# Optimization experiments

Measured on AMD Instinct MI355X. Metric: run time of the kernel, lower is better.

The kernel has to match this reference:

```python
import jax, jax.numpy as jnp
import numpy as np

N, E, F, H, S, L, B = 20000, 320000, 64, 256, 32, 128, 16
TAU = 1.0
EPS = 1e-9


def _glorot(k, i, o):
    return (jax.random.normal(k, (i, o), jnp.float32) / np.sqrt(i)).astype(jnp.float32)


def _mlp3(h, w1, b1, w2, b2, w3, b3):
    h = jax.nn.relu(h @ w1 + b1)
    h = jax.nn.relu(h @ w2 + b2)
    return h @ w3 + b3


def _gnn_layer(x, src, dst, w1, b1, w2, b2, w3, b3):
    # PyG: x_i = x[dst] (target), x_j = x[src] (source); aggregate 'add' at target
    m = _mlp3(jnp.concatenate([x[dst], x[src]], axis=1), w1, b1, w2, b2, w3, b3)  # [E, H]
    return jax.ops.segment_sum(m, dst, num_segments=N)  # [N, H]


def _layer_norm(x, g, b):
    mu = x.mean(-1, keepdims=True)
    var = ((x - mu) ** 2).mean(-1, keepdims=True)
    return (x - mu) * jax.lax.rsqrt(var + 1e-5) * g + b


def setup_inputs() -> dict:
    key = jax.random.key(0)
    ks = jax.random.split(key, 32)
    d = {
        'x': jax.random.normal(ks[0], (N, F), jnp.float32),
        'u': jax.random.uniform(ks[1], (N, S), jnp.float32, minval=1e-6, maxval=1.0 - 1e-6),
        'edge_index': jax.random.randint(ks[2], (2, E), 0, N, jnp.int32),
        'batch': jnp.sort(jax.random.randint(ks[3], (N,), 0, B, jnp.int32)),
        # gnn1 MLP: 2F -> H -> H -> H
        'g1w1': _glorot(ks[4], 2 * F, H), 'g1b1': jnp.zeros((H,), jnp.float32),
        'g1w2': _glorot(ks[5], H, H),     'g1b2': jnp.zeros((H,), jnp.float32),
        'g1w3': _glorot(ks[6], H, H),     'g1b3': jnp.zeros((H,), jnp.float32),
        'ln1g': jnp.ones((H,), jnp.float32), 'ln1b': jnp.zeros((H,), jnp.float32),
        # gnn2 MLP: 2H -> H -> H -> H
        'g2w1': _glorot(ks[7], 2 * H, H), 'g2b1': jnp.zeros((H,), jnp.float32),
        'g2w2': _glorot(ks[8], H, H),     'g2b2': jnp.zeros((H,), jnp.float32),
        'g2w3': _glorot(ks[9], H, H),     'g2b3': jnp.zeros((H,), jnp.float32),
        'ln2g': jnp.ones((H,), jnp.float32), 'ln2b': jnp.zeros((H,), jnp.float32),
        # assignment MLP: H -> H -> S
        'aw1': _glorot(ks[10], H, H), 'ab1': jnp.zeros((H,), jnp.float32),
        'aw2': _glorot(ks[11], H, S), 'ab2': jnp.zeros((S,), jnp.float32),
        # output MLP: H -> H -> L
        'ow1': _glorot(ks[12], H, H), 'ob1': jnp.zeros((H,), jnp.float32),
        'ow2': _glorot(ks[13], H, L), 'ob2': jnp.zeros((L,), jnp.float32),
    }
    return d


def reference(x, u, edge_index, batch,
              g1w1, g1b1, g1w2, g1b2, g1w3, g1b3, ln1g, ln1b,
              g2w1, g2b1, g2w2, g2b2, g2w3, g2b3, ln2g, ln2b,
              aw1, ab1, aw2, ab2, ow1, ob1, ow2, ob2):
    src, dst = edge_index[0], edge_index[1]
    x = _layer_norm(jax.nn.relu(_gnn_layer(x, src, dst, g1w1, g1b1, g1w2, g1b2, g1w3, g1b3)), ln1g, ln1b)
    x = _layer_norm(jax.nn.relu(_gnn_layer(x, src, dst, g2w1, g2b1, g2w2, g2b2, g2w3, g2b3)), ln2g, ln2b)
    # Hierarchical pooling with Gumbel-softmax (soft, tau=1.0); u is the uniform noise
    logits = jax.nn.relu(x @ aw1 + ab1) @ aw2 + ab2  # [N, S]
    g = -jnp.log(-jnp.log(u + EPS) + EPS)
    s = jax.nn.softmax((logits + g) / TAU, axis=-1)  # [N, S]
    entropy = -jnp.mean(jnp.sum(s * jnp.log(s + EPS), axis=1))
    avg_s = s.mean(axis=0)
    diversity = jnp.sum(avg_s * jnp.log(avg_s + EPS))
    assign_loss = entropy + diversity
    xe = x[:, None, :] * s[:, :, None]  # [N, S, H]
    pooled = jax.ops.segment_sum(xe, batch, num_segments=B)  # [B, S, H]
    latent = jax.nn.relu(pooled @ ow1 + ob1) @ ow2 + ob2  # [B, S, L]
    return (latent, s, assign_loss)
```

## Files before the change

### kernel.cpp

```cpp
#include <hip/hip_runtime.h>
#include <stdint.h>

#define NN 20000
#define NE 320000
#define NBATCH 16
#define NTILE 2500

typedef short short8 __attribute__((ext_vector_type(8)));
typedef float f32x4  __attribute__((ext_vector_type(4)));

__device__ __forceinline__ unsigned short f2bf(float f) {
  union { float f; unsigned u; } v; v.f = f;
  unsigned r = v.u + 0x7FFFu + ((v.u >> 16) & 1u);
  return (unsigned short)(r >> 16);
}
__device__ __forceinline__ float bf2f(unsigned short h) {
  union { unsigned u; float f; } v; v.u = ((unsigned)h) << 16;
  return v.f;
}
__device__ __forceinline__ float bf2fs(short h) { return bf2f((unsigned short)h); }

__device__ __forceinline__ unsigned cvt_pk_bf16(float lo, float hi) {
  unsigned r;
  asm("v_cvt_pk_bf16_f32 %0, %1, %2" : "=v"(r) : "v"(lo), "v"(hi));
  return r;
}

#define HOFF(e, k) (((e) << 8) + (((((k) >> 3) ^ ((e) & 7)) << 3) + ((k) & 7)))
#define HK(e, k, KT) ((e) * (KT) + (((((k) >> 3) ^ ((e) & 7)) << 3) + ((k) & 7)))

struct TD { const float* s; unsigned short* d; int R, C, r0, ld; };
struct TDs { TD t[13]; };

__global__ void wprep(TDs all, const int* __restrict__ dstI, int* __restrict__ deg) {
  if (blockIdx.y == 13) {
    int stride = gridDim.x * blockDim.x;
    for (int e = blockIdx.x * blockDim.x + threadIdx.x; e < NE; e += stride)
      atomicAdd(&deg[dstI[e]], 1);
    return;
  }
  TD td = all.t[blockIdx.y];
  int stride = gridDim.x * blockDim.x;
  int i0 = blockIdx.x * blockDim.x + threadIdx.x;
  if (td.ld == 0) {
    for (int i = i0; i < td.R; i += stride) td.d[i] = f2bf(td.s[i]);
  } else {
    int total = td.R * td.C;
    for (int i = i0; i < total; i += stride) {
      int c = i / td.R;
      int r = i - c * td.R;
      td.d[i] = f2bf(td.s[(size_t)(td.r0 + r) * td.ld + c]);
    }
  }
}

__global__ void scan_bounds(const int* __restrict__ deg, int* __restrict__ rowstart,
                            int* __restrict__ cursor, const int* __restrict__ batch,
                            int* __restrict__ bstart,
                            const float* __restrict__ g1b1, const float* __restrict__ g2b1,
                            float* __restrict__ b1cat1, float* __restrict__ b1cat2) {
  if (blockIdx.x == 0) {
    __shared__ int part[256];
    int t = threadIdx.x;
    int c0 = t * 80; if (c0 > NN) c0 = NN;
    int c1 = c0 + 80; if (c1 > NN) c1 = NN;
    int s = 0;
    for (int i = c0; i < c1; ++i) s += deg[i];
    part[t] = s;
    __syncthreads();
    if (t == 0) {
      int run = 0;
      for (int i = 0; i < 256; ++i) { int v = part[i]; part[i] = run; run += v; }
    }
    __syncthreads();
    int run = part[t];
    for (int i = c0; i < c1; ++i) { rowstart[i] = run; cursor[i] = run; run += deg[i]; }
    if (t == 255) rowstart[NN] = run;
  } else if (blockIdx.x == 80) {
    int t = threadIdx.x;
    b1cat1[t] = g1b1[t]; b1cat1[256 + t] = 0.f;
    b1cat2[t] = g2b1[t]; b1cat2[256 + t] = 0.f;
  } else {
    int n = (blockIdx.x - 1) * 256 + threadIdx.x;
    if (n >= NN) return;
    int bn = batch[n];
    if (n == 0) {
      for (int b2 = 0; b2 <= bn; ++b2) bstart[b2] = 0;
    } else {
      int bp = batch[n - 1];
      for (int b2 = bp + 1; b2 <= bn; ++b2) bstart[b2] = n;
    }
    if (n == NN - 1) {
      for (int b2 = bn + 1; b2 <= NBATCH; ++b2) bstart[b2] = NN;
    }
  }
}

__global__ void fillcsr(const int* __restrict__ srcI, const int* __restrict__ dstI,
                        int* __restrict__ cursor, int* __restrict__ sSrc,
                        int* __restrict__ sDst) {
  int e = blockIdx.x * 256 + threadIdx.x;
  if (e < NE) {
    int d = dstI[e];
    int slot = atomicAdd(&cursor[d], 1);
    sDst[slot] = d;
    sSrc[slot] = srcI[e];
  }
}

template <int KT>
__global__ __launch_bounds__(512, 4) void gemmTs(
    const unsigned short* __restrict__ WT, const unsigned short* __restrict__ In,
    const float* __restrict__ bias, unsigned short* __restrict__ Out,
    int M, int Nout, int ldo) {
  __shared__ __align__(16) unsigned short h[128 * KT];
  const int tid = threadIdx.x;
  const int rb0 = blockIdx.y * 128;
  {
    int r = tid & 127;
    int rg = rb0 + r; if (rg >= M) rg = M - 1;
    const unsigned short* src = In + (size_t)rg * KT + (tid >> 7) * (KT / 4);
    int c0 = (tid >> 7) * (KT / 4);
#pragma unroll
    for (int i = 0; i < KT / 32; ++i) {
      short8 v = *(const short8*)(src + i * 8);
      *(short8*)&h[HK(r, c0 + i * 8, KT)] = v;
    }
  }
  __syncthreads();

  const int lane = tid & 63, w = tid >> 6;
  const int wf = w >> 1, we = w & 1;
  const int l15 = lane & 15, q = lane >> 4;
  const int fb = blockIdx.x * 256 + wf * 64;
  const int rb = rb0 + we * 64;
  f32x4 acc[4][4] = {};
  const short8 zz = {0, 0, 0, 0, 0, 0, 0, 0};
  for (int kc = 0; kc < KT; kc += 32) {
    short8 a[4], bq[4];
#pragma unroll
    for (int i = 0; i < 4; ++i) {
      if (fb + i * 16 < Nout)
        a[i] = *(const short8*)(WT + (size_t)(fb + i * 16 + l15) * KT + kc + q * 8);
      else
        a[i] = zz;
      bq[i] = *(const short8*)&h[HK(we * 64 + i * 16 + l15, kc + q * 8, KT)];
    }
#pragma unroll
    for (int i = 0; i < 4; ++i)
#pragma unroll
      for (int j = 0; j < 4; ++j)
        acc[i][j] = __builtin_amdgcn_mfma_f32_16x16x32_bf16(a[i], bq[j], acc[i][j], 0, 0, 0);
  }
#pragma unroll
  for (int i = 0; i < 4; ++i) {
    int f0 = fb + i * 16 + q * 4;
    if (f0 >= Nout) continue;
    float4 bs = make_float4(0.f, 0.f, 0.f, 0.f);
    if (bias) bs = *(const float4*)(bias + f0);
#pragma unroll
    for (int j = 0; j < 4; ++j) {
      int r = rb + j * 16 + l15;
      if (r >= M) continue;
      uint2 o = make_uint2(cvt_pk_bf16(acc[i][j][0] + bs.x, acc[i][j][1] + bs.y),
                           cvt_pk_bf16(acc[i][j][2] + bs.z, acc[i][j][3] + bs.w));
      *(uint2*)(Out + (size_t)r * ldo + f0) = o;
    }
  }
}

__global__ __launch_bounds__(512, 4) void edge_h2agg(
    const unsigned short* __restrict__ PQ, const int* __restrict__ sSrc,
    const int* __restrict__ sDst,
    const unsigned short* __restrict__ W2T, const float* __restrict__ b2,
    int* __restrict__ segcnt, int* __restrict__ segbuf, float* __restrict__ agg) {
  __shared__ __align__(16) unsigned short h[128 * 256];
  const int tid = threadIdx.x;
  const int e0 = blockIdx.x * 128;

  {
    int r = tid & 127;
    int c0 = (tid >> 7) * 64;
    int dn = sDst[e0 + r];
    int sn = sSrc[e0 + r];
    const unsigned short* pd = PQ + (size_t)dn * 512 + c0;
    const unsigned short* ps = PQ + (size_t)sn * 512 + 256 + c0;
#pragma unroll
    for (int i = 0; i < 8; ++i) {
      short8 dv = *(const short8*)(pd + i * 8);
      short8 sv = *(const short8*)(ps + i * 8);
      float a0 = fmaxf(bf2fs(dv[0]) + bf2fs(sv[0]), 0.f);
      float a1 = fmaxf(bf2fs(dv[1]) + bf2fs(sv[1]), 0.f);
      float a2 = fmaxf(bf2fs(dv[2]) + bf2fs(sv[2]), 0.f);
      float a3 = fmaxf(bf2fs(dv[3]) + bf2fs(sv[3]), 0.f);
      float a4 = fmaxf(bf2fs(dv[4]) + bf2fs(sv[4]), 0.f);
      float a5 = fmaxf(bf2fs(dv[5]) + bf2fs(sv[5]), 0.f);
      float a6 = fmaxf(bf2fs(dv[6]) + bf2fs(sv[6]), 0.f);
      float a7 = fmaxf(bf2fs(dv[7]) + bf2fs(sv[7]), 0.f);
      uint4 o = make_uint4(cvt_pk_bf16(a0, a1), cvt_pk_bf16(a2, a3),
                           cvt_pk_bf16(a4, a5), cvt_pk_bf16(a6, a7));
      *(uint4*)&h[HOFF(r, c0 + i * 8)] = o;
    }
  }
  __syncthreads();

  const int lane = tid & 63, w = tid >> 6;
  const int wf = w >> 1, we = w & 1;
  const int l15 = lane & 15, q = lane >> 4;
  const int fb = wf * 64, eb = we * 64;
  f32x4 acc[4][4];

#pragma unroll
  for (int i = 0; i < 4; ++i)
#pragma unroll
    for (int j = 0; j < 4; ++j) { f32x4 z = {0.f, 0.f, 0.f, 0.f}; acc[i][j] = z; }
  for (int kc = 0; kc < 256; kc += 32) {
    short8 a[4], bq[4];
#pragma unroll
    for (int i = 0; i < 4; ++i)
      a[i] = *(const short8*)(W2T + (size_t)(fb + i * 16 + l15) * 256 + kc + q * 8);
#pragma unroll
    for (int j = 0; j < 4; ++j)
      bq[j] = *(const short8*)&h[HOFF(eb + j * 16 + l15, kc + q * 8)];
#pragma unroll
    for (int i = 0; i < 4; ++i)
#pragma unroll
      for (int j = 0; j < 4; ++j)
        acc[i][j] = __builtin_amdgcn_mfma_f32_16x16x32_bf16(a[i], bq[j], acc[i][j], 0, 0, 0);
  }
  __syncthreads();
#pragma unroll
  for (int i = 0; i < 4; ++i) {
    int f0 = fb + i * 16 + q * 4;
    float4 bs = *(const float4*)(b2 + f0);
#pragma unroll
    for (int j = 0; j < 4; ++j) {
      int e = eb + j * 16 + l15;
      float v0 = fmaxf(acc[i][j][0] + bs.x, 0.f);
      float v1 = fmaxf(acc[i][j][1] + bs.y, 0.f);
      float v2 = fmaxf(acc[i][j][2] + bs.z, 0.f);
      float v3 = fmaxf(acc[i][j][3] + bs.w, 0.f);
      uint2 o = make_uint2(cvt_pk_bf16(v0, v1), cvt_pk_bf16(v2, v3));
      *(uint2*)&h[HOFF(e, f0)] = o;
    }
  }
  if (tid < 128) {
    int d0 = sDst[e0 + tid];
    bool flag = (tid == 0) || (sDst[e0 + tid - 1] != d0);
    if (flag) {
      int idx = atomicAdd(&segcnt[blockIdx.x], 1);
      segbuf[blockIdx.x * 128 + idx] = tid;
    }
  }
  __syncthreads();

  {
    int cnt = segcnt[blockIdx.x];
    int f4 = (tid & 63) * 4;
    int sg = tid >> 6;
    const int* sb = segbuf + blockIdx.x * 128;
    for (int k = sg; k < cnt; k += 8) {
      int start = sb[k];
      int end = 128;
      for (int j2 = 0; j2 < cnt; ++j2) {
        int v = sb[j2];
        if (v > start && v < end) end = v;
      }
      int node = sDst[e0 + start];
      float s0 = 0.f, s1 = 0.f, s2 = 0.f, s3 = 0.f;
      for (int rr = start; rr < end; ++rr) {
        ushort4 v = *(const ushort4*)&h[HOFF(rr, f4)];
        s0 += bf2f(v.x); s1 += bf2f(v.y); s2 += bf2f(v.z); s3 += bf2f(v.w);
      }
      float* pr = agg + (size_t)node * 256 + f4;
      if (start == 0 || end == 128) {
        atomicAdd(pr + 0, s0); atomicAdd(pr + 1, s1);
        atomicAdd(pr + 2, s2); atomicAdd(pr + 3, s3);
      } else {
        *(float4*)pr = make_float4(s0, s1, s2, s3);
      }
    }
  }
}

__global__ __launch_bounds__(512, 4) void node_gemm(
    const unsigned short* __restrict__ W3T, const float* __restrict__ aggH2,
    const float* __restrict__ b3, const int* __restrict__ deg,
    float* __restrict__ outm) {
  __shared__ __align__(16) unsigned short h[128 * 256];
  const int tid = threadIdx.x;
  const int rb0 = blockIdx.x * 128;
  {
    int r = tid & 127;
    int rg = rb0 + r; if (rg >= NN) rg = NN - 1;
    int c0 = (tid >> 7) * 64;
    const float* src = aggH2 + (size_t)rg * 256 + c0;
#pragma unroll
    for (int i = 0; i < 8; ++i) {
      float4 lo = *(const float4*)(src + i * 8);
      float4 hi = *(const float4*)(src + i * 8 + 4);
      uint4 o = make_uint4(cvt_pk_bf16(lo.x, lo.y), cvt_pk_bf16(lo.z, lo.w),
                           cvt_pk_bf16(hi.x, hi.y), cvt_pk_bf16(hi.z, hi.w));
      *(uint4*)&h[HOFF(r, c0 + i * 8)] = o;
    }
  }
  __syncthreads();

  const int lane = tid & 63, w = tid >> 6;
  const int wf = w >> 1, we = w & 1;
  const int l15 = lane & 15, q = lane >> 4;
  const int fb = wf * 64;
  const int rb = rb0 + we * 64;
  f32x4 acc[4][4] = {};
  for (int kc = 0; kc < 256; kc += 32) {
    short8 a[4], bq[4];
#pragma unroll
    for (int i = 0; i < 4; ++i) {
      a[i] = *(const short8*)(W3T + (size_t)(fb + i * 16 + l15) * 256 + kc + q * 8);
      bq[i] = *(const short8*)&h[HOFF(we * 64 + i * 16 + l15, kc + q * 8)];
    }
#pragma unroll
    for (int i = 0; i < 4; ++i)
#pragma unroll
      for (int j = 0; j < 4; ++j)
        acc[i][j] = __builtin_amdgcn_mfma_f32_16x16x32_bf16(a[i], bq[j], acc[i][j], 0, 0, 0);
  }
#pragma unroll
  for (int i = 0; i < 4; ++i) {
    int f0 = fb + i * 16 + q * 4;
    float4 b3v = *(const float4*)(b3 + f0);
#pragma unroll
    for (int j = 0; j < 4; ++j) {
      int r = rb + j * 16 + l15;
      if (r >= NN) continue;
      float dg = (float)deg[r];
      *(float4*)(outm + (size_t)r * 256 + f0) =
          make_float4(acc[i][j][0] + dg * b3v.x, acc[i][j][1] + dg * b3v.y,
                      acc[i][j][2] + dg * b3v.z, acc[i][j][3] + dg * b3v.w);
    }
  }
}

__global__ void relu_ln(const float* __restrict__ agg, const float* __restrict__ g,
                        const float* __restrict__ b, unsigned short* __restrict__ out) {
  int row = blockIdx.x * 4 + (threadIdx.x >> 6);
  int lane = threadIdx.x & 63;
  if (row >= NN) return;
  float4 v = *(const float4*)(agg + (size_t)row * 256 + lane * 4);
  v.x = fmaxf(v.x, 0.f); v.y = fmaxf(v.y, 0.f); v.z = fmaxf(v.z, 0.f); v.w = fmaxf(v.w, 0.f);
  float s = v.x + v.y + v.z + v.w;
  float sq = v.x * v.x + v.y * v.y + v.z * v.z + v.w * v.w;
  for (int off = 32; off >= 1; off >>= 1) {
    s += __shfl_xor(s, off);
    sq += __shfl_xor(sq, off);
  }
  float mu = s * (1.f / 256.f);
  float var = sq * (1.f / 256.f) - mu * mu;
  float rs = rsqrtf(var + 1e-5f);
  float4 gg = *(const float4*)(g + lane * 4);
  float4 bb = *(const float4*)(b + lane * 4);
  ushort4 o;
  o.x = f2bf((v.x - mu) * rs * gg.x + bb.x);
  o.y = f2bf((v.y - mu) * rs * gg.y + bb.y);
  o.z = f2bf((v.z - mu) * rs * gg.z + bb.z);
  o.w = f2bf((v.w - mu) * rs * gg.w + bb.w);
  *(ushort4*)(out + (size_t)row * 256 + lane * 4) = o;
}

__global__ __launch_bounds__(512, 4) void assign_gumbel(
    const unsigned short* __restrict__ x2b, const unsigned short* __restrict__ aw1T,
    const float* __restrict__ ab1, const unsigned short* __restrict__ aw2T,
    const float* __restrict__ ab2, const float* __restrict__ u,
    float* __restrict__ sf, float* __restrict__ entacc, float* __restrict__ avgacc) {
  __shared__ __align__(16) unsigned short sh[64 * 256];
  __shared__ float sh_logit[64 * 33];
  __shared__ float lavg[32];
  __shared__ float lent;
  const int tid = threadIdx.x;
  const int n0 = blockIdx.x * 64;
  if (tid < 32) lavg[tid] = 0.f;
  if (tid == 0) lent = 0.f;

  const int lane = tid & 63, w = tid >> 6;
  const int l15 = lane & 15, q = lane >> 4;

  {
    const int wf = w >> 1, we = w & 1;
    const int fb = wf * 64, eb = we * 32;
    f32x4 acc[4][2];
#pragma unroll
    for (int i = 0; i < 4; ++i)
#pragma unroll
      for (int j = 0; j < 2; ++j) { f32x4 z = {0.f, 0.f, 0.f, 0.f}; acc[i][j] = z; }
    for (int kc = 0; kc < 256; kc += 32) {
      short8 a[4], bq[2];
#pragma unroll
      for (int i = 0; i < 4; ++i)
        a[i] = *(const short8*)(aw1T + (size_t)(fb + i * 16 + l15) * 256 + kc + q * 8);
#pragma unroll
      for (int j = 0; j < 2; ++j) {
        int rr = n0 + eb + j * 16 + l15;
        if (rr >= NN) rr = NN - 1;
        bq[j] = *(const short8*)(x2b + (size_t)rr * 256 + kc + q * 8);
      }
#pragma unroll
      for (int i = 0; i < 4; ++i)
#pragma unroll
        for (int j = 0; j < 2; ++j)
          acc[i][j] = __builtin_amdgcn_mfma_f32_16x16x32_bf16(a[i], bq[j], acc[i][j], 0, 0, 0);
    }
#pragma unroll
    for (int i = 0; i < 4; ++i) {
      int f0 = fb + i * 16 + q * 4;
      float4 bs = *(const float4*)(ab1 + f0);
#pragma unroll
      for (int j = 0; j < 2; ++j) {
        int e = eb + j * 16 + l15;
        ushort4 o;
        o.x = f2bf(fmaxf(acc[i][j][0] + bs.x, 0.f));
        o.y = f2bf(fmaxf(acc[i][j][1] + bs.y, 0.f));
        o.z = f2bf(fmaxf(acc[i][j][2] + bs.z, 0.f));
        o.w = f2bf(fmaxf(acc[i][j][3] + bs.w, 0.f));
        *(ushort4*)&sh[HOFF(e, f0)] = o;
      }
    }
  }
  __syncthreads();

  {
    const int rg = w & 3, fg = w >> 2;
    if (fg < 2) {
      f32x4 acc = {0.f, 0.f, 0.f, 0.f};
      for (int kc = 0; kc < 256; kc += 32) {
        short8 a = *(const short8*)(aw2T + (size_t)(fg * 16 + l15) * 256 + kc + q * 8);
        short8 bq = *(const short8*)&sh[HOFF(rg * 16 + l15, kc + q * 8)];
        acc = __builtin_amdgcn_mfma_f32_16x16x32_bf16(a, bq, acc, 0, 0, 0);
      }
      int rowL = rg * 16 + l15;
#pragma unroll
      for (int t2 = 0; t2 < 4; ++t2) {
        int f = fg * 16 + q * 4 + t2;
        sh_logit[rowL * 33 + f] = acc[t2] + ab2[f];
      }
    }
  }
  __syncthreads();

  if (tid < 256) {
    int rowL = tid >> 2, sub = tid & 3;
    int n = n0 + rowL;
    if (n < NN) {
      int j0 = sub * 8;
      float z[8];
      float4 u0 = *(const float4*)(u + (size_t)n * 32 + j0);
      float4 u1 = *(const float4*)(u + (size_t)n * 32 + j0 + 4);
      float uu[8] = {u0.x, u0.y, u0.z, u0.w, u1.x, u1.y, u1.z, u1.w};
      float m = -1e30f;
#pragma unroll
      for (int j = 0; j < 8; ++j) {
        z[j] = sh_logit[rowL * 33 + j0 + j] - logf(-logf(uu[j] + 1e-9f) + 1e-9f);
        m = fmaxf(m, z[j]);
      }
      m = fmaxf(m, __shfl_xor(m, 1));
      m = fmaxf(m, __shfl_xor(m, 2));
      float sum = 0.f;
#pragma unroll
      for (int j = 0; j < 8; ++j) { z[j] = expf(z[j] - m); sum += z[j]; }
      sum += __shfl_xor(sum, 1);
      sum += __shfl_xor(sum, 2);
      float inv = 1.f / sum;
      float ent = 0.f;
      float so[8];
#pragma unroll
      for (int j = 0; j < 8; ++j) {
        float sj = z[j] * inv;
        so[j] = sj;
        ent += sj * logf(sj + 1e-9f);
        atomicAdd(&lavg[j0 + j], sj);
      }
      *(float4*)(sf + (size_t)n * 32 + j0) = make_float4(so[0], so[1], so[2], so[3]);
      *(float4*)(sf + (size_t)n * 32 + j0 + 4) = make_float4(so[4], so[5], so[6], so[7]);
      ent += __shfl_xor(ent, 1);
      ent += __shfl_xor(ent, 2);
      if (sub == 0) atomicAdd(&lent, ent);
    }
  }
  __syncthreads();
  if (tid < 32) atomicAdd(&avgacc[tid], lavg[tid]);
  if (tid == 0) atomicAdd(entacc, lent);
}

__global__ __launch_bounds__(512, 4) void pool_part(
    const unsigned short* __restrict__ x2b, const float* __restrict__ sf,
    const int* __restrict__ bstart, float* __restrict__ part) {
  const int b = blockIdx.x, ci = blockIdx.y;
  const int n0b = bstart[b], n1b = bstart[b + 1];
  const int t = threadIdx.x;
  const int si = t >> 4;
  const int h0 = (t & 15) * 16;
  float acc[16];
#pragma unroll
  for (int k = 0; k < 16; ++k) acc[k] = 0.f;
  for (int nst = n0b + ci * 64; nst < n1b; nst += 16 * 64) {
    int nend = (nst + 64 < n1b) ? nst + 64 : n1b;
    for (int n = nst; n < nend; ++n) {
      float sv = sf[(size_t)n * 32 + si];
      const unsigned short* xr = x2b + (size_t)n * 256 + h0;
      short8 x0 = *(const short8*)xr;
      short8 x1 = *(const short8*)(xr + 8);
#pragma unroll
      for (int j = 0; j < 8; ++j) acc[j] = fmaf(sv, bf2fs(x0[j]), acc[j]);
#pragma unroll
      for (int j = 0; j < 8; ++j) acc[8 + j] = fmaf(sv, bf2fs(x1[j]), acc[8 + j]);
    }
  }
  float* pp = part + (((size_t)b * 16 + ci) << 13) + si * 256 + h0;
#pragma unroll
  for (int k = 0; k < 16; k += 4)
    *(float4*)(pp + k) = make_float4(acc[k], acc[k + 1], acc[k + 2], acc[k + 3]);
}

__global__ void pool_reduce(const float* __restrict__ part, float* __restrict__ pooled) {
  int g = blockIdx.x * 256 + threadIdx.x;
  int b = g >> 13, rem = g & 8191;
  const float* p = part + (((size_t)b * 16) << 13) + rem;
  float s = 0.f;
#pragma unroll
  for (int c = 0; c < 16; ++c) s += p[(size_t)c << 13];
  pooled[g] = s;
}

__global__ __launch_bounds__(512, 4) void out_mlp(
    const float* __restrict__ pooled, const unsigned short* __restrict__ ow1T,
    const float* __restrict__ ob1, const unsigned short* __restrict__ ow2T,
    const float* __restrict__ ob2, float* __restrict__ latent,
    const float* __restrict__ accs, float* __restrict__ outloss) {
  __shared__ __align__(16) unsigned short sh[64 * 256];
  const int tid = threadIdx.x;
  const int n0 = blockIdx.x * 64;
  const int lane = tid & 63, w = tid >> 6;
  const int l15 = lane & 15, q = lane >> 4;

  if (blockIdx.x == 0 && tid < 64) {
    float d = 0.f;
    if (tid < 32) {
      float a = accs[16 + tid] * (1.f / NN);
      d = a * logf(a + 1e-9f);
    }
    for (int off = 32; off >= 1; off >>= 1) d += __shfl_xor(d, off);
    if (tid == 0) outloss[0] = -accs[0] * (1.f / NN) + d;
  }

  {
    const int wf = w >> 1, we = w & 1;
    const int fb = wf * 64, eb = we * 32;
    f32x4 acc[4][2];
#pragma unroll
    for (int i = 0; i < 4; ++i)
#pragma unroll
      for (int j = 0; j < 2; ++j) { f32x4 z = {0.f, 0.f, 0.f, 0.f}; acc[i][j] = z; }
    for (int kc = 0; kc < 256; kc += 32) {
      short8 a[4], bq[2];
#pragma unroll
      for (int i = 0; i < 4; ++i)
        a[i] = *(const short8*)(ow1T + (size_t)(fb + i * 16 + l15) * 256 + kc + q * 8);
#pragma unroll
      for (int j = 0; j < 2; ++j) {
        int rr = n0 + eb + j * 16 + l15;
        const float* pr = pooled + (size_t)rr * 256 + kc + q * 8;
        float4 lo = *(const float4*)pr;
        float4 hi = *(const float4*)(pr + 4);
        short8 o;
        o[0] = (short)f2bf(lo.x); o[1] = (short)f2bf(lo.y);
        o[2] = (short)f2bf(lo.z); o[3] = (short)f2bf(lo.w);
        o[4] = (short)f2bf(hi.x); o[5] = (short)f2bf(hi.y);
        o[6] = (short)f2bf(hi.z); o[7] = (short)f2bf(hi.w);
        bq[j] = o;
      }
#pragma unroll
      for (int i = 0; i < 4; ++i)
#pragma unroll
        for (int j = 0; j < 2; ++j)
          acc[i][j] = __builtin_amdgcn_mfma_f32_16x16x32_bf16(a[i], bq[j], acc[i][j], 0, 0, 0);
    }
#pragma unroll
    for (int i = 0; i < 4; ++i) {
      int f0 = fb + i * 16 + q * 4;
      float4 bs = *(const float4*)(ob1 + f0);
#pragma unroll
      for (int j = 0; j < 2; ++j) {
        int e = eb + j * 16 + l15;
        ushort4 o;
        o.x = f2bf(fmaxf(acc[i][j][0] + bs.x, 0.f));
        o.y = f2bf(fmaxf(acc[i][j][1] + bs.y, 0.f));
        o.z = f2bf(fmaxf(acc[i][j][2] + bs.z, 0.f));
        o.w = f2bf(fmaxf(acc[i][j][3] + bs.w, 0.f));
        *(ushort4*)&sh[HOFF(e, f0)] = o;
      }
    }
  }
  __syncthreads();

  {
    const int wf = w >> 1, we = w & 1;
    const int fb = wf * 32, eb = we * 32;
    f32x4 acc[2][2];
#pragma unroll
    for (int i = 0; i < 2; ++i)
#pragma unroll
      for (int j = 0; j < 2; ++j) { f32x4 z = {0.f, 0.f, 0.f, 0.f}; acc[i][j] = z; }
    for (int kc = 0; kc < 256; kc += 32) {
      short8 a[2], bq[2];
#pragma unroll
      for (int i = 0; i < 2; ++i)
        a[i] = *(const short8*)(ow2T + (size_t)(fb + i * 16 + l15) * 256 + kc + q * 8);
#pragma unroll
      for (int j = 0; j < 2; ++j)
        bq[j] = *(const short8*)&sh[HOFF(eb + j * 16 + l15, kc + q * 8)];
#pragma unroll
      for (int i = 0; i < 2; ++i)
#pragma unroll
        for (int j = 0; j < 2; ++j)
          acc[i][j] = __builtin_amdgcn_mfma_f32_16x16x32_bf16(a[i], bq[j], acc[i][j], 0, 0, 0);
    }
#pragma unroll
    for (int i = 0; i < 2; ++i) {
      int f0 = fb + i * 16 + q * 4;
      float4 bs = *(const float4*)(ob2 + f0);
#pragma unroll
      for (int j = 0; j < 2; ++j) {
        int rr = n0 + eb + j * 16 + l15;
        *(float4*)(latent + (size_t)rr * 128 + f0) =
            make_float4(acc[i][j][0] + bs.x, acc[i][j][1] + bs.y,
                        acc[i][j][2] + bs.z, acc[i][j][3] + bs.w);
      }
    }
  }
}

extern "C" void kernel_launch(void* const* d_in, const int* in_sizes, int n_in,
                              void* d_out, int out_size, void* d_ws, size_t ws_size,
                              hipStream_t stream) {
  (void)in_sizes; (void)n_in; (void)out_size; (void)ws_size;
  const float* x = (const float*)d_in[0];
  const float* u = (const float*)d_in[1];
  const int* ei = (const int*)d_in[2];
  const int* batch = (const int*)d_in[3];
  const float* g1w1 = (const float*)d_in[4];
  const float* g1b1 = (const float*)d_in[5];
  const float* g1w2 = (const float*)d_in[6];
  const float* g1b2 = (const float*)d_in[7];
  const float* g1w3 = (const float*)d_in[8];
  const float* g1b3 = (const float*)d_in[9];
  const float* ln1g = (const float*)d_in[10];
  const float* ln1b = (const float*)d_in[11];
  const float* g2w1 = (const float*)d_in[12];
  const float* g2b1 = (const float*)d_in[13];
  const float* g2w2 = (const float*)d_in[14];
  const float* g2b2 = (const float*)d_in[15];
  const float* g2w3 = (const float*)d_in[16];
  const float* g2b3 = (const float*)d_in[17];
  const float* ln2g = (const float*)d_in[18];
  const float* ln2b = (const float*)d_in[19];
  const float* aw1 = (const float*)d_in[20];
  const float* ab1 = (const float*)d_in[21];
  const float* aw2 = (const float*)d_in[22];
  const float* ab2 = (const float*)d_in[23];
  const float* ow1 = (const float*)d_in[24];
  const float* ob1 = (const float*)d_in[25];
  const float* ow2 = (const float*)d_in[26];
  const float* ob2 = (const float*)d_in[27];
  const int* srcI = ei;
  const int* dstI = ei + NE;

  char* wp = (char*)d_ws;
  size_t off = 0;
  auto alloc = [&](size_t bytes) {
    void* p = wp + off;
    off += (bytes + 255) & ~(size_t)255;
    return p;
  };
  unsigned short* W1catT = (unsigned short*)alloc((size_t)512 * 64 * 2);
  unsigned short* W2catT = (unsigned short*)alloc((size_t)512 * 256 * 2);
  unsigned short* g1w2T = (unsigned short*)alloc((size_t)256 * 256 * 2);
  unsigned short* g1w3T = (unsigned short*)alloc((size_t)256 * 256 * 2);
  unsigned short* g2w2T = (unsigned short*)alloc((size_t)256 * 256 * 2);
  unsigned short* g2w3T = (unsigned short*)alloc((size_t)256 * 256 * 2);
  unsigned short* aw1T = (unsigned short*)alloc((size_t)256 * 256 * 2);
  unsigned short* aw2T = (unsigned short*)alloc((size_t)32 * 256 * 2);
  unsigned short* ow1T = (unsigned short*)alloc((size_t)256 * 256 * 2);
  unsigned short* ow2T = (unsigned short*)alloc((size_t)128 * 256 * 2);
  unsigned short* xb = (unsigned short*)alloc((size_t)NN * 64 * 2);
  unsigned short* PQ = (unsigned short*)alloc((size_t)NN * 512 * 2);
  unsigned short* x1b = (unsigned short*)alloc((size_t)NN * 256 * 2);
  unsigned short* x2b = (unsigned short*)alloc((size_t)NN * 256 * 2);
  int* bstart = (int*)alloc(32 * 4);
  int* cursor = (int*)alloc((size_t)NN * 4);
  int* rowstart = (int*)alloc((size_t)(NN + 1) * 4);
  int* sSrc = (int*)alloc((size_t)NE * 4);
  int* sDst = (int*)alloc((size_t)NE * 4);
  int* segbuf = (int*)alloc((size_t)2 * NTILE * 128 * 4);
  float* b1cat1 = (float*)alloc(512 * 4);
  float* b1cat2 = (float*)alloc(512 * 4);
  char* zbase = (char*)(wp + off);
  float* accs = (float*)alloc(64 * 4);
  float* pooled = (float*)alloc((size_t)512 * 256 * 4);
  int* deg = (int*)alloc((size_t)NN * 4);
  int* segcnt = (int*)alloc((size_t)2 * NTILE * 4);
  float* agg1 = (float*)alloc((size_t)NN * 256 * 4);
  float* agg2 = (float*)alloc((size_t)NN * 256 * 4);
  size_t zbytes = (size_t)((char*)(wp + off) - zbase);

  float* aggm = (float*)PQ;
  float* poolpart = agg1;

  float* out_f = (float*)d_out;
  float* out_latent = out_f;
  float* out_s = out_f + 65536;
  float* out_loss = out_f + 65536 + 640000;

  TDs tds;
  tds.t[0] = {g1w1, W1catT, 64, 256, 0, 256};
  tds.t[1] = {g1w1, W1catT + 256 * 64, 64, 256, 64, 256};
  tds.t[2] = {g1w2, g1w2T, 256, 256, 0, 256};
  tds.t[3] = {g1w3, g1w3T, 256, 256, 0, 256};
  tds.t[4] = {g2w1, W2catT, 256, 256, 0, 256};
  tds.t[5] = {g2w1, W2catT + 256 * 256, 256, 256, 256, 256};
  tds.t[6] = {g2w2, g2w2T, 256, 256, 0, 256};
  tds.t[7] = {g2w3, g2w3T, 256, 256, 0, 256};
  tds.t[8] = {aw1, aw1T, 256, 256, 0, 256};
  tds.t[9] = {aw2, aw2T, 256, 32, 0, 32};
  tds.t[10] = {ow1, ow1T, 256, 256, 0, 256};
  tds.t[11] = {ow2, ow2T, 256, 128, 0, 128};
  tds.t[12] = {x, xb, NN * 64, 1, 0, 0};

  (void)hipMemsetAsync(zbase, 0, zbytes, stream);
  wprep<<<dim3(128, 14), 256, 0, stream>>>(tds, dstI, deg);

  scan_bounds<<<dim3(81), 256, 0, stream>>>(deg, rowstart, cursor, batch, bstart,
                                            g1b1, g2b1, b1cat1, b1cat2);
  fillcsr<<<dim3(1250), 256, 0, stream>>>(srcI, dstI, cursor, sSrc, sDst);

  gemmTs<64><<<dim3(2, 157), 512, 0, stream>>>(W1catT, xb, b1cat1, PQ, NN, 512, 512);
  edge_h2agg<<<dim3(NTILE), 512, 0, stream>>>(PQ, sSrc, sDst, g1w2T, g1b2,
                                              segcnt, segbuf, agg1);
  node_gemm<<<dim3(157), 512, 0, stream>>>(g1w3T, agg1, g1b3, deg, aggm);
  relu_ln<<<dim3(5000), 256, 0, stream>>>(aggm, ln1g, ln1b, x1b);

  gemmTs<256><<<dim3(2, 157), 512, 0, stream>>>(W2catT, x1b, b1cat2, PQ, NN, 512, 512);
  edge_h2agg<<<dim3(NTILE), 512, 0, stream>>>(PQ, sSrc, sDst, g2w2T, g2b2,
                                              segcnt + NTILE, segbuf + (size_t)NTILE * 128, agg2);
  node_gemm<<<dim3(157), 512, 0, stream>>>(g2w3T, agg2, g2b3, deg, aggm);
  relu_ln<<<dim3(5000), 256, 0, stream>>>(aggm, ln2g, ln2b, x2b);

  assign_gumbel<<<dim3(313), 512, 0, stream>>>(x2b, aw1T, ab1, aw2T, ab2, u,
                                               out_s, accs, accs + 16);

  pool_part<<<dim3(16, 16), 512, 0, stream>>>(x2b, out_s, bstart, poolpart);
  pool_reduce<<<dim3(512), 256, 0, stream>>>(poolpart, pooled);

  out_mlp<<<dim3(8), 512, 0, stream>>>(pooled, ow1T, ob1, ow2T, ob2, out_latent,
                                       accs, out_loss);
}
```

Before: 679.4 us.

## Process two edge tiles per block with register-resident weights and prefetched gathers

The edge MLP+aggregation kernel now handles two 128-edge tiles per block. It keeps the W2 weight fragments in registers across both tiles and prefetches the next tile's PQ gathers while the current tile runs its MFMA. Segment bookkeeping moves from global atomics and buffers into shared memory, which removes the segcnt/segbuf allocations. The cost is much higher register pressure (128 VGPRs of weights plus the prefetch registers), which may lower occupancy under launch_bounds(512,4) or cause spills.

```diff
diff --git a/kernel.cpp b/kernel.cpp
--- a/kernel.cpp
+++ b/kernel.cpp
@@ -4,7 +4,8 @@
 #define NN 20000
 #define NE 320000
 #define NBATCH 16
-#define NTILE 2500
+#define EB_TPB 2
+#define EB_GRID 1250
 
 typedef short short8 __attribute__((ext_vector_type(8)));
 typedef float f32x4  __attribute__((ext_vector_type(4)));
@@ -173,113 +174,137 @@
     const unsigned short* __restrict__ PQ, const int* __restrict__ sSrc,
     const int* __restrict__ sDst,
     const unsigned short* __restrict__ W2T, const float* __restrict__ b2,
-    int* __restrict__ segcnt, int* __restrict__ segbuf, float* __restrict__ agg) {
+    float* __restrict__ agg) {
   __shared__ __align__(16) unsigned short h[128 * 256];
+  __shared__ int seg_s[129];
   const int tid = threadIdx.x;
-  const int e0 = blockIdx.x * 128;
-
-  {
-    int r = tid & 127;
-    int c0 = (tid >> 7) * 64;
-    int dn = sDst[e0 + r];
-    int sn = sSrc[e0 + r];
-    const unsigned short* pd = PQ + (size_t)dn * 512 + c0;
-    const unsigned short* ps = PQ + (size_t)sn * 512 + 256 + c0;
-#pragma unroll
-    for (int i = 0; i < 8; ++i) {
-      short8 dv = *(const short8*)(pd + i * 8);
-      short8 sv = *(const short8*)(ps + i * 8);
-      float a0 = fmaxf(bf2fs(dv[0]) + bf2fs(sv[0]), 0.f);
-      float a1 = fmaxf(bf2fs(dv[1]) + bf2fs(sv[1]), 0.f);
-      float a2 = fmaxf(bf2fs(dv[2]) + bf2fs(sv[2]), 0.f);
-      float a3 = fmaxf(bf2fs(dv[3]) + bf2fs(sv[3]), 0.f);
-      float a4 = fmaxf(bf2fs(dv[4]) + bf2fs(sv[4]), 0.f);
-      float a5 = fmaxf(bf2fs(dv[5]) + bf2fs(sv[5]), 0.f);
-      float a6 = fmaxf(bf2fs(dv[6]) + bf2fs(sv[6]), 0.f);
-      float a7 = fmaxf(bf2fs(dv[7]) + bf2fs(sv[7]), 0.f);
-      uint4 o = make_uint4(cvt_pk_bf16(a0, a1), cvt_pk_bf16(a2, a3),
-                           cvt_pk_bf16(a4, a5), cvt_pk_bf16(a6, a7));
-      *(uint4*)&h[HOFF(r, c0 + i * 8)] = o;
-    }
-  }
-  __syncthreads();
-
   const int lane = tid & 63, w = tid >> 6;
   const int wf = w >> 1, we = w & 1;
   const int l15 = lane & 15, q = lane >> 4;
   const int fb = wf * 64, eb = we * 64;
-  f32x4 acc[4][4];
-
+  const int r = tid & 127;
+  const int c0 = (tid >> 7) * 64;
+  const int e0 = blockIdx.x * (128 * EB_TPB);
+
+  short8 wa[4][8];
 #pragma unroll
   for (int i = 0; i < 4; ++i)
 #pragma unroll
-    for (int j = 0; j < 4; ++j) { f32x4 z = {0.f, 0.f, 0.f, 0.f}; acc[i][j] = z; }
-  for (int kc = 0; kc < 256; kc += 32) {
-    short8 a[4], bq[4];
+    for (int kk = 0; kk < 8; ++kk)
+      wa[i][kk] = *(const short8*)(W2T + (size_t)(fb + i * 16 + l15) * 256 + kk * 32 + q * 8);
+
+  short8 dv[8], sv[8];
+  {
+    int dn = sDst[e0 + r], sn = sSrc[e0 + r];
+    const unsigned short* pd = PQ + (size_t)dn * 512 + c0;
+    const unsigned short* ps = PQ + (size_t)sn * 512 + 256 + c0;
+#pragma unroll
+    for (int i = 0; i < 8; ++i) {
+      dv[i] = *(const short8*)(pd + i * 8);
+      sv[i] = *(const short8*)(ps + i * 8);
+    }
+  }
+
+  for (int t = 0; t < EB_TPB; ++t) {
+    const int te0 = e0 + t * 128;
+#pragma unroll
+    for (int i = 0; i < 8; ++i) {
+      float a0 = fmaxf(bf2fs(dv[i][0]) + bf2fs(sv[i][0]), 0.f);
+      float a1 = fmaxf(bf2fs(dv[i][1]) + bf2fs(sv[i][1]), 0.f);
+      float a2 = fmaxf(bf2fs(dv[i][2]) + bf2fs(sv[i][2]), 0.f);
+      float a3 = fmaxf(bf2fs(dv[i][3]) + bf2fs(sv[i][3]), 0.f);
+      float a4 = fmaxf(bf2fs(dv[i][4]) + bf2fs(sv[i][4]), 0.f);
+      float a5 = fmaxf(bf2fs(dv[i][5]) + bf2fs(sv[i][5]), 0.f);
+      float a6 = fmaxf(bf2fs(dv[i][6]) + bf2fs(sv[i][6]), 0.f);
+      float a7 = fmaxf(bf2fs(dv[i][7]) + bf2fs(sv[i][7]), 0.f);
+      uint4 o = make_uint4(cvt_pk_bf16(a0, a1), cvt_pk_bf16(a2, a3),
+                           cvt_pk_bf16(a4, a5), cvt_pk_bf16(a6, a7));
+      *(uint4*)&h[HOFF(r, c0 + i * 8)] = o;
+    }
+    if (t + 1 < EB_TPB) {
+      int dn = sDst[te0 + 128 + r], sn = sSrc[te0 + 128 + r];
+      const unsigned short* pd = PQ + (size_t)dn * 512 + c0;
+      const unsigned short* ps = PQ + (size_t)sn * 512 + 256 + c0;
+#pragma unroll
+      for (int i = 0; i < 8; ++i) {
+        dv[i] = *(const short8*)(pd + i * 8);
+        sv[i] = *(const short8*)(ps + i * 8);
+      }
+    }
+    asm volatile("" ::: "memory");
+    __syncthreads();
+    if (tid == 0) seg_s[128] = 0;
+
+    f32x4 acc[4][4];
 #pragma unroll
     for (int i = 0; i < 4; ++i)
-      a[i] = *(const short8*)(W2T + (size_t)(fb + i * 16 + l15) * 256 + kc + q * 8);
-#pragma unroll
-    for (int j = 0; j < 4; ++j)
-      bq[j] = *(const short8*)&h[HOFF(eb + j * 16 + l15, kc + q * 8)];
-#pragma unroll
-    for (int i = 0; i < 4; ++i)
+#pragma unroll
+      for (int j = 0; j < 4; ++j) { f32x4 z = {0.f, 0.f, 0.f, 0.f}; acc[i][j] = z; }
+#pragma unroll
+    for (int kk = 0; kk < 8; ++kk) {
+      short8 bq[4];
 #pragma unroll
       for (int j = 0; j < 4; ++j)
-        acc[i][j] = __builtin_amdgcn_mfma_f32_16x16x32_bf16(a[i], bq[j], acc[i][j], 0, 0, 0);
-  }
-  __syncthreads();
-#pragma unroll
-  for (int i = 0; i < 4; ++i) {
-    int f0 = fb + i * 16 + q * 4;
-    float4 bs = *(const float4*)(b2 + f0);
-#pragma unroll
-    for (int j = 0; j < 4; ++j) {
-      int e = eb + j * 16 + l15;
-      float v0 = fmaxf(acc[i][j][0] + bs.x, 0.f);
-      float v1 = fmaxf(acc[i][j][1] + bs.y, 0.f);
-      float v2 = fmaxf(acc[i][j][2] + bs.z, 0.f);
-      float v3 = fmaxf(acc[i][j][3] + bs.w, 0.f);
-      uint2 o = make_uint2(cvt_pk_bf16(v0, v1), cvt_pk_bf16(v2, v3));
-      *(uint2*)&h[HOFF(e, f0)] = o;
-    }
-  }
-  if (tid < 128) {
-    int d0 = sDst[e0 + tid];
-    bool flag = (tid == 0) || (sDst[e0 + tid - 1] != d0);
-    if (flag) {
-      int idx = atomicAdd(&segcnt[blockIdx.x], 1);
-      segbuf[blockIdx.x * 128 + idx] = tid;
-    }
-  }
-  __syncthreads();
-
-  {
-    int cnt = segcnt[blockIdx.x];
-    int f4 = (tid & 63) * 4;
-    int sg = tid >> 6;
-    const int* sb = segbuf + blockIdx.x * 128;
-    for (int k = sg; k < cnt; k += 8) {
-      int start = sb[k];
-      int end = 128;
-      for (int j2 = 0; j2 < cnt; ++j2) {
-        int v = sb[j2];
-        if (v > start && v < end) end = v;
-      }
-      int node = sDst[e0 + start];
-      float s0 = 0.f, s1 = 0.f, s2 = 0.f, s3 = 0.f;
-      for (int rr = start; rr < end; ++rr) {
-        ushort4 v = *(const ushort4*)&h[HOFF(rr, f4)];
-        s0 += bf2f(v.x); s1 += bf2f(v.y); s2 += bf2f(v.z); s3 += bf2f(v.w);
-      }
-      float* pr = agg + (size_t)node * 256 + f4;
-      if (start == 0 || end == 128) {
-        atomicAdd(pr + 0, s0); atomicAdd(pr + 1, s1);
-        atomicAdd(pr + 2, s2); atomicAdd(pr + 3, s3);
-      } else {
-        *(float4*)pr = make_float4(s0, s1, s2, s3);
-      }
-    }
+        bq[j] = *(const short8*)&h[HOFF(eb + j * 16 + l15, kk * 32 + q * 8)];
+#pragma unroll
+      for (int i = 0; i < 4; ++i)
+#pragma unroll
+        for (int j = 0; j < 4; ++j)
+          acc[i][j] = __builtin_amdgcn_mfma_f32_16x16x32_bf16(wa[i][kk], bq[j], acc[i][j], 0, 0, 0);
+    }
+    __syncthreads();
+#pragma unroll
+    for (int i = 0; i < 4; ++i) {
+      int f0 = fb + i * 16 + q * 4;
+      float4 bs = *(const float4*)(b2 + f0);
+#pragma unroll
+      for (int j = 0; j < 4; ++j) {
+        int e = eb + j * 16 + l15;
+        float v0 = fmaxf(acc[i][j][0] + bs.x, 0.f);
+        float v1 = fmaxf(acc[i][j][1] + bs.y, 0.f);
+        float v2 = fmaxf(acc[i][j][2] + bs.z, 0.f);
+        float v3 = fmaxf(acc[i][j][3] + bs.w, 0.f);
+        uint2 o = make_uint2(cvt_pk_bf16(v0, v1), cvt_pk_bf16(v2, v3));
+        *(uint2*)&h[HOFF(e, f0)] = o;
+      }
+    }
+    if (tid < 128) {
+      int d0 = sDst[te0 + tid];
+      bool flag = (tid == 0) || (sDst[te0 + tid - 1] != d0);
+      if (flag) {
+        int idx = atomicAdd(&seg_s[128], 1);
+        seg_s[idx] = tid;
+      }
+    }
+    __syncthreads();
+
+    {
+      int cnt = seg_s[128];
+      int f4 = (tid & 63) * 4;
+      int sg = tid >> 6;
+      for (int k = sg; k < cnt; k += 8) {
+        int start = seg_s[k];
+        int end = 128;
+        for (int j2 = 0; j2 < cnt; ++j2) {
+          int v = seg_s[j2];
+          if (v > start && v < end) end = v;
+        }
+        int node = sDst[te0 + start];
+        float s0 = 0.f, s1 = 0.f, s2 = 0.f, s3 = 0.f;
+        for (int rr = start; rr < end; ++rr) {
+          ushort4 v = *(const ushort4*)&h[HOFF(rr, f4)];
+          s0 += bf2f(v.x); s1 += bf2f(v.y); s2 += bf2f(v.z); s3 += bf2f(v.w);
+        }
+        float* pr = agg + (size_t)node * 256 + f4;
+        if (start == 0 || end == 128) {
+          atomicAdd(pr + 0, s0); atomicAdd(pr + 1, s1);
+          atomicAdd(pr + 2, s2); atomicAdd(pr + 3, s3);
+        } else {
+          *(float4*)pr = make_float4(s0, s1, s2, s3);
+        }
+      }
+    }
+    if (t + 1 < EB_TPB) __syncthreads();
   }
 }
 
@@ -699,14 +724,12 @@
   int* rowstart = (int*)alloc((size_t)(NN + 1) * 4);
   int* sSrc = (int*)alloc((size_t)NE * 4);
   int* sDst = (int*)alloc((size_t)NE * 4);
-  int* segbuf = (int*)alloc((size_t)2 * NTILE * 128 * 4);
   float* b1cat1 = (float*)alloc(512 * 4);
   float* b1cat2 = (float*)alloc(512 * 4);
   char* zbase = (char*)(wp + off);
   float* accs = (float*)alloc(64 * 4);
   float* pooled = (float*)alloc((size_t)512 * 256 * 4);
   int* deg = (int*)alloc((size_t)NN * 4);
-  int* segcnt = (int*)alloc((size_t)2 * NTILE * 4);
   float* agg1 = (float*)alloc((size_t)NN * 256 * 4);
   float* agg2 = (float*)alloc((size_t)NN * 256 * 4);
   size_t zbytes = (size_t)((char*)(wp + off) - zbase);
@@ -742,14 +765,12 @@
   fillcsr<<<dim3(1250), 256, 0, stream>>>(srcI, dstI, cursor, sSrc, sDst);
 
   gemmTs<64><<<dim3(2, 157), 512, 0, stream>>>(W1catT, xb, b1cat1, PQ, NN, 512, 512);
-  edge_h2agg<<<dim3(NTILE), 512, 0, stream>>>(PQ, sSrc, sDst, g1w2T, g1b2,
-                                              segcnt, segbuf, agg1);
+  edge_h2agg<<<dim3(EB_GRID), 512, 0, stream>>>(PQ, sSrc, sDst, g1w2T, g1b2, agg1);
   node_gemm<<<dim3(157), 512, 0, stream>>>(g1w3T, agg1, g1b3, deg, aggm);
   relu_ln<<<dim3(5000), 256, 0, stream>>>(aggm, ln1g, ln1b, x1b);
 
   gemmTs<256><<<dim3(2, 157), 512, 0, stream>>>(W2catT, x1b, b1cat2, PQ, NN, 512, 512);
-  edge_h2agg<<<dim3(NTILE), 512, 0, stream>>>(PQ, sSrc, sDst, g2w2T, g2b2,
-                                              segcnt + NTILE, segbuf + (size_t)NTILE * 128, agg2);
+  edge_h2agg<<<dim3(EB_GRID), 512, 0, stream>>>(PQ, sSrc, sDst, g2w2T, g2b2, agg2);
   node_gemm<<<dim3(157), 512, 0, stream>>>(g2w3T, agg2, g2b3, deg, aggm);
   relu_ln<<<dim3(5000), 256, 0, stream>>>(aggm, ln2g, ln2b, x2b);
 
```

New measurement: 1.283 ms. 88.9% more time.
